# Optimization experiments

Hardware: AMD Instinct MI355X
Metric: run time of the kernel (lower is better)

## Reference

```python
import jax, jax.numpy as jnp
import numpy as np

B, T, C, H = 2, 2048, 1024, 16
HD = C // H  # head dim = 64


def setup_inputs() -> dict:
    key = jax.random.key(0)
    k0, k1, k2 = jax.random.split(key, 3)
    x = jax.random.normal(k0, (B, T, C), jnp.float32)
    W_attn = jax.random.normal(k1, (C, 3 * C), jnp.float32) * 0.02
    b_attn = jnp.zeros((3 * C,), jnp.float32)
    W_proj = jax.random.normal(k2, (C, C), jnp.float32) * 0.02
    b_proj = jnp.zeros((C,), jnp.float32)
    # causal mask, broadcast over (B, H) like torch masked_fill(~mask)
    attn_mask = jnp.tril(jnp.ones((T, T), dtype=bool))[None, None]
    return {"x": x, "W_attn": W_attn, "b_attn": b_attn,
            "W_proj": W_proj, "b_proj": b_proj, "attn_mask": attn_mask}


def _rotate_half(x):
    # interleaved rotate_half as in rotary-embedding-torch: (x1,x2)->(-x2,x1)
    x1 = x[..., 0::2]
    x2 = x[..., 1::2]
    return jnp.stack((-x2, x1), axis=-1).reshape(x.shape)


def _apply_rope(x):
    # x: [B, H, T, HD]
    hd = x.shape[-1]
    t = x.shape[-2]
    inv_freq = 1.0 / (10000.0 ** (jnp.arange(0, hd, 2, dtype=jnp.float32) / hd))
    freqs = jnp.arange(t, dtype=jnp.float32)[:, None] * inv_freq[None, :]  # [T, HD/2]
    freqs = jnp.repeat(freqs, 2, axis=-1)  # [T, HD], interleaved
    return x * jnp.cos(freqs) + _rotate_half(x) * jnp.sin(freqs)


def reference(x, W_attn, b_attn, W_proj, b_proj, attn_mask):
    Bb, Tt, Cc = x.shape
    qkv = x @ W_attn + b_attn                     # [B, T, 3C]
    q, k, v = jnp.split(qkv, 3, axis=-1)

    def to_heads(z):
        return z.reshape(Bb, Tt, H, HD).transpose(0, 2, 1, 3)  # [B, H, T, HD]

    q, k, v = to_heads(q), to_heads(k), to_heads(v)
    q = _apply_rope(q)
    k = _apply_rope(k)

    scale = 1.0 / jnp.sqrt(jnp.float32(HD))
    att = jnp.einsum('bhqd,bhkd->bhqk', q, k) * scale  # [B, H, T, T]
    att = jnp.where(attn_mask, att, jnp.float32(-10000.0))
    att = jax.nn.softmax(att, axis=-1)
    # dropout = 0.0 (eval): identity
    y = jnp.einsum('bhqk,bhkd->bhqd', att, v)           # [B, H, T, HD]
    y = y.transpose(0, 2, 1, 3).reshape(Bb, Tt, Cc)
    return y @ W_proj + b_proj
```

## Files before the change

### kernel.cpp

```cpp
#include <hip/hip_runtime.h>

#define B_ 2
#define T_ 2048
#define C_ 1024
#define H_ 16
#define HD_ 64

typedef unsigned short u16;
typedef unsigned int u32;
typedef __attribute__((ext_vector_type(8))) short short8;
typedef __attribute__((ext_vector_type(4))) float f32x4;
typedef __attribute__((ext_vector_type(2))) u32 uint2v;
typedef __attribute__((ext_vector_type(4))) u32 uint4v;

typedef __attribute__((address_space(1))) const void* as1cv;
typedef __attribute__((address_space(3))) void* as3v;

__device__ __forceinline__ u16 f2bf(float x){
  union { float f; u32 u; } v; v.f = x;
  u32 r = v.u + 0x7fffu + ((v.u >> 16) & 1u);
  return (u16)(r >> 16);
}
__device__ __forceinline__ float bf2f(u16 h){
  union { u32 u; float f; } v; v.u = ((u32)h) << 16;
  return v.f;
}
__device__ __forceinline__ u32 cvt_pk_bf16(float lo, float hi){
  u32 r;
  asm("v_cvt_pk_bf16_f32 %0, %1, %2" : "=v"(r) : "v"(lo), "v"(hi));
  return r;
}
__device__ __forceinline__ void gl_lds16(const u16* src, u16* dst){
  __builtin_amdgcn_global_load_lds((as1cv)src, (as3v)dst, 16, 0, 0);
}

__global__ void k_prep(const float* __restrict__ x, u16* __restrict__ xb,
                       const float* __restrict__ Wa, u16* __restrict__ WaT,
                       const float* __restrict__ Wp, u16* __restrict__ WpT)
{
  __shared__ float tile[32][33];
  int b = blockIdx.x;
  int tid = threadIdx.x;
  if (b < 4096){
    int i = b*256 + tid;
    f32x4 v = ((const f32x4*)x)[i];
    uint2v o;
    o.x = (u32)f2bf(v.x) | ((u32)f2bf(v.y) << 16);
    o.y = (u32)f2bf(v.z) | ((u32)f2bf(v.w) << 16);
    ((uint2v*)xb)[i] = o;
    return;
  }
  const float* in; u16* out; int R, Cc, c0, r0;
  if (b < 7168){
    int bb = b - 4096;
    in = Wa; out = WaT; R = 1024; Cc = 3072;
    c0 = (bb % 96) * 32; r0 = (bb / 96) * 32;
  } else {
    int bb = b - 7168;
    in = Wp; out = WpT; R = 1024; Cc = 1024;
    c0 = (bb & 31) * 32; r0 = (bb >> 5) * 32;
  }
  int tx = tid & 31, ty = tid >> 5;
#pragma unroll
  for (int ii = 0; ii < 4; ++ii)
    tile[ty + ii*8][tx] = in[(size_t)(r0 + ty + ii*8) * Cc + c0 + tx];
  __syncthreads();
#pragma unroll
  for (int ii = 0; ii < 4; ++ii)
    out[(size_t)(c0 + ty + ii*8) * R + r0 + tx] = f2bf(tile[tx][ty + ii*8]);
}

__global__ __launch_bounds__(256, 3)
void k_gemm0(const u16* __restrict__ A, const u16* __restrict__ Bt,
             const float* __restrict__ bias, u16* __restrict__ Qh,
             u16* __restrict__ Kh, u16* __restrict__ vt,
             int M, int N, int K)
{
  __shared__ u16 As[128*64];
  __shared__ u16 Bs[128*64];
  int nwg = gridDim.x;
  int cpx = nwg >> 3;
  int bid = blockIdx.x;
  int wg = (bid & 7) * cpx + (bid >> 3);
  int ntn = N >> 7;
  int m0 = (wg / ntn) << 7, n0 = (wg % ntn) << 7;
  int tid = threadIdx.x;
  int lane = tid & 63, w = tid >> 6;
  int c = lane & 15, g = lane >> 4;
  int wr = w >> 1, wc = w & 1;
  int c7 = c & 7;

  f32x4 z4 = {0.f,0.f,0.f,0.f};
  f32x4 acc[4][4];
#pragma unroll
  for (int i=0;i<4;++i)
#pragma unroll
    for (int j=0;j<4;++j) acc[i][j] = z4;

  u16* dstA = As + ((tid & 0xC0) << 3);
  u16* dstB = Bs + ((tid & 0xC0) << 3);
  int rowS[4], soffS[4];
#pragma unroll
  for (int it=0; it<4; ++it){
    int ch = it*256 + tid;
    rowS[it] = ch >> 3;
    soffS[it] = (((ch & 7) ^ (rowS[it] & 7)) << 3);
  }

  for (int k0 = 0; k0 < K; k0 += 64){
#pragma unroll
    for (int it = 0; it < 4; ++it)
      gl_lds16(A + (size_t)(m0+rowS[it])*K + k0 + soffS[it], dstA + it*2048);
#pragma unroll
    for (int it = 0; it < 4; ++it)
      gl_lds16(Bt + (size_t)(n0+rowS[it])*K + k0 + soffS[it], dstB + it*2048);
    __syncthreads();
#pragma unroll
    for (int ks = 0; ks < 2; ++ks){
      short8 af[4], bf[4];
      int sx = ((ks*4 + g) ^ c7) << 3;
#pragma unroll
      for (int i=0;i<4;++i)
        af[i] = *(const short8*)(As + (wr*64 + i*16 + c)*64 + sx);
#pragma unroll
      for (int j=0;j<4;++j)
        bf[j] = *(const short8*)(Bs + (wc*64 + j*16 + c)*64 + sx);
#pragma unroll
      for (int i=0;i<4;++i)
#pragma unroll
        for (int j=0;j<4;++j)
          acc[i][j] = __builtin_amdgcn_mfma_f32_16x16x32_bf16(af[i], bf[j], acc[i][j], 0, 0, 0);
    }
    __syncthreads();
  }

  if (n0 >= 2048){
#pragma unroll
    for (int i=0;i<4;++i){
      int rowb = m0 + wr*64 + i*16 + g*4;
      int bb = rowb >> 11, t0 = rowb & 2047;
#pragma unroll
      for (int j=0;j<4;++j){
        int col = n0 + wc*64 + j*16 + c;
        float bv = bias[col];
        int vc = col - 2048;
        int hh = vc >> 6, d = vc & 63;
        uint2v o;
        o.x = (u32)f2bf(acc[i][j].x + bv) | ((u32)f2bf(acc[i][j].y + bv) << 16);
        o.y = (u32)f2bf(acc[i][j].z + bv) | ((u32)f2bf(acc[i][j].w + bv) << 16);
        *(uint2v*)(vt + ((size_t)((bb*16 + hh)*64 + d))*2048 + t0) = o;
      }
    }
  } else {
    bool isQ = (n0 < 1024);
    u16* dsth = isQ ? Qh : Kh;
    int colb = isQ ? n0 : (n0 - 1024);
    float qsc = isQ ? 0.180336880f : 1.0f;
    float sgn = (c & 1) ? 1.f : -1.f;
#pragma unroll
    for (int nf=0; nf<4; ++nf){
      int scol = colb + wc*64 + nf*16 + c;
      int hh = scol >> 6, d = scol & 63;
      int ip = (d >> 1);
      float invr = exp2f((float)(-ip) * 0.4152410118609203f) * 0.15915494309f;
      float bv = bias[n0 + wc*64 + nf*16 + c];
      u16* base = dsth + (size_t)hh*2048*64 + d;
#pragma unroll
      for (int mf=0; mf<4; ++mf){
#pragma unroll
        for (int r=0; r<4; ++r){
          int row = m0 + wr*64 + mf*16 + g*4 + r;
          int t = row & 2047, b = row >> 11;
          float v = acc[mf][nf][r] + bv;
          float p = __shfl_xor(v, 1);
          float th = (float)t * invr;
          float fr = th - floorf(th);
          float sn = __builtin_amdgcn_sinf(fr);
          float cs = __builtin_amdgcn_cosf(fr);
          float y = (v*cs + p*sn*sgn) * qsc;
          base[((size_t)b*16*2048 + t)*64] = f2bf(y);
        }
      }
    }
  }
}

__global__ __launch_bounds__(256, 3)
void k_gemmp(const u16* __restrict__ A, const u16* __restrict__ Bt,
             const float* __restrict__ bias, float* __restrict__ outf)
{
  __shared__ u16 LDSG[24576];
  const int K = 1024, N = 1024;
  int nwg = gridDim.x;
  int cpx = nwg >> 3;
  int bid = blockIdx.x;
  int wg = (bid & 7) * cpx + (bid >> 3);
  int m0 = (wg >> 3) << 6, n0 = (wg & 7) << 7;
  int tid = threadIdx.x;
  int lane = tid & 63, w = tid >> 6;
  int c = lane & 15, g = lane >> 4;
  int wr = w >> 1, wc = w & 1;
  int c7 = c & 7;

  f32x4 z4 = {0.f,0.f,0.f,0.f};
  f32x4 acc[2][4];
#pragma unroll
  for (int i=0;i<2;++i)
#pragma unroll
    for (int j=0;j<4;++j) acc[i][j] = z4;

  int rowA[2], slotA[2], dstA[2];
#pragma unroll
  for (int it=0; it<2; ++it){
    int ch = it*256 + tid;
    rowA[it] = ch >> 3;
    slotA[it] = (((ch & 7) ^ (rowA[it] & 7)) << 3);
    dstA[it] = it*2048 + ((tid & 0xC0) << 3);
  }
  int rowB[4], slotB[4], dstB[4];
#pragma unroll
  for (int it=0; it<4; ++it){
    int ch = it*256 + tid;
    rowB[it] = ch >> 3;
    slotB[it] = (((ch & 7) ^ (rowB[it] & 7)) << 3);
    dstB[it] = 8192 + it*2048 + ((tid & 0xC0) << 3);
  }
  const u16* Abase = A + (size_t)m0*K;
  const u16* Bbase = Bt + (size_t)n0*K;

#pragma unroll
  for (int it=0; it<2; ++it)
    gl_lds16(Abase + (size_t)rowA[it]*K + slotA[it], LDSG + dstA[it]);
#pragma unroll
  for (int it=0; it<4; ++it)
    gl_lds16(Bbase + (size_t)rowB[it]*K + slotB[it], LDSG + dstB[it]);
  __syncthreads();

  const int nk = K >> 6;
  for (int kt = 0; kt < nk; ++kt){
    int cur = kt & 1;
    if (kt + 1 < nk){
      int k1 = (kt + 1) << 6;
      int nb = cur ^ 1;
#pragma unroll
      for (int it=0; it<2; ++it)
        gl_lds16(Abase + (size_t)rowA[it]*K + k1 + slotA[it], LDSG + nb*4096 + dstA[it]);
#pragma unroll
      for (int it=0; it<4; ++it)
        gl_lds16(Bbase + (size_t)rowB[it]*K + k1 + slotB[it], LDSG + nb*8192 + dstB[it]);
    }
    const u16* As = LDSG + cur*4096;
    const u16* Bs = LDSG + 8192 + cur*8192;
#pragma unroll
    for (int ks = 0; ks < 2; ++ks){
      short8 af[2], bf[4];
      int sx = ((ks*4 + g) ^ c7) << 3;
#pragma unroll
      for (int i=0;i<2;++i)
        af[i] = *(const short8*)(As + (wr*32 + i*16 + c)*64 + sx);
#pragma unroll
      for (int j=0;j<4;++j)
        bf[j] = *(const short8*)(Bs + (wc*64 + j*16 + c)*64 + sx);
#pragma unroll
      for (int i=0;i<2;++i)
#pragma unroll
        for (int j=0;j<4;++j)
          acc[i][j] = __builtin_amdgcn_mfma_f32_16x16x32_bf16(af[i], bf[j], acc[i][j], 0, 0, 0);
    }
    __syncthreads();
  }

#pragma unroll
  for (int i=0;i<2;++i){
#pragma unroll
    for (int j=0;j<4;++j){
      int col = n0 + wc*64 + j*16 + c;
      float bv = bias[col];
#pragma unroll
      for (int r=0;r<4;++r){
        int row = m0 + wr*32 + i*16 + g*4 + r;
        outf[(size_t)row*N + col] = acc[i][j][r] + bv;
      }
    }
  }
}

__global__ __launch_bounds__(256, 3)
void k_attn(const u16* __restrict__ Qh, const u16* __restrict__ Kh,
            const u16* __restrict__ Vt, u16* __restrict__ Pb,
            float* __restrict__ lp)
{
  __shared__ u16 KV[4*4096];
  __shared__ u16 Ps[4*32*64];

  int bid = blockIdx.x;
  int qt, ck, bh, l2nsp;
  if (bid < 1536){
    qt = 15 - (bid >> 7); ck = (bid >> 5) & 3; bh = bid & 31; l2nsp = 2;
  } else if (bid < 1728){
    int x = bid - 1536;
    qt = 3 - (x >> 6); ck = (x >> 5) & 1; bh = x & 31; l2nsp = 1;
  } else {
    qt = 0; ck = 0; bh = (bid - 1728) & 31; l2nsp = 0;
  }
  int q0 = qt << 7;
  int tid = threadIdx.x, lane = tid & 63, w = tid >> 6;
  int c = lane & 15, g = lane >> 4;
  int q0w = q0 + w*32;
  int nt = (qt + 1) << 1;
  int t0 = (nt * ck) >> l2nsp;
  int t1 = (nt * (ck + 1)) >> l2nsp;

  const u16* Kbase = Kh + (size_t)bh * T_ * 64;
  const u16* Vbase = Vt + (size_t)bh * 64 * T_;
  const u16* Qbase = Qh + (size_t)bh * T_ * 64;

  short8 qf[2][2];
#pragma unroll
  for (int qs=0;qs<2;++qs)
#pragma unroll
    for (int ks=0;ks<2;++ks)
      qf[qs][ks] = *(const short8*)(Qbase + (size_t)(q0w + qs*16 + c)*64 + ks*32 + g*8);

  f32x4 z4 = {0.f,0.f,0.f,0.f};
  f32x4 acc[2][4];
#pragma unroll
  for (int qs=0;qs<2;++qs)
#pragma unroll
    for (int ds=0;ds<4;++ds) acc[qs][ds] = z4;
  float psum[2] = {0.f, 0.f};

  char* PsB = (char*)Ps + w*4096;

  int row2[2], soff2[2];
  u16* dst0[2];
#pragma unroll
  for (int it=0; it<2; ++it){
    int ch = it*256 + tid;
    row2[it] = ch >> 3;
    int slot = ch & 7;
    soff2[it] = (slot ^ (row2[it] & 7)) << 3;
    dst0[it] = KV + ((it*256 + (tid & 0xC0)) << 3);
  }

  {
    int kv0 = t0 << 6;
#pragma unroll
    for (int it=0; it<2; ++it){
      gl_lds16(Kbase + (size_t)(kv0 + row2[it])*64 + soff2[it], dst0[it]);
      gl_lds16(Vbase + (size_t)row2[it]*T_ + kv0 + soff2[it], dst0[it] + 2*4096);
    }
  }
  __syncthreads();

  for (int t = t0; t < t1; ++t){
    int cur = (t - t0) & 1;
    int kv0 = t << 6;
    if (t + 1 < t1){
      int kvn = kv0 + 64;
      int nxt = cur ^ 1;
#pragma unroll
      for (int it=0; it<2; ++it){
        gl_lds16(Kbase + (size_t)(kvn + row2[it])*64 + soff2[it], dst0[it] + nxt*4096);
        gl_lds16(Vbase + (size_t)row2[it]*T_ + kvn + soff2[it], dst0[it] + (2+nxt)*4096);
      }
    }

    if (kv0 <= q0w + 31){
      const char* KsC = (const char*)(KV + cur*4096);
      const char* VsC = (const char*)(KV + (2+cur)*4096);

      f32x4 st[4][2];
#pragma unroll
      for (int kv=0;kv<4;++kv)
#pragma unroll
        for (int qs=0;qs<2;++qs) st[kv][qs] = z4;

#pragma unroll
      for (int ks=0;ks<2;++ks){
        short8 kf[4];
#pragma unroll
        for (int kv=0;kv<4;++kv){
          int row = kv*16 + c;
          kf[kv] = *(const short8*)(KsC + row*128 + (((ks*4+g) ^ (row&7)) << 4));
        }
#pragma unroll
        for (int kv=0;kv<4;++kv)
#pragma unroll
          for (int qs=0;qs<2;++qs)
            st[kv][qs] = __builtin_amdgcn_mfma_f32_16x16x32_bf16(kf[kv], qf[qs][ks], st[kv][qs], 0, 0, 0);
      }

      if (kv0 + 63 > q0w){
#pragma unroll
        for (int kv=0;kv<4;++kv)
#pragma unroll
          for (int qs=0;qs<2;++qs)
#pragma unroll
            for (int r=0;r<4;++r){
              int kvi = kv0 + kv*16 + g*4 + r;
              int qi = q0w + qs*16 + c;
              if (kvi > qi) st[kv][qs][r] = -INFINITY;
            }
      }

#pragma unroll
      for (int qs=0;qs<2;++qs){
        float s01 = 0.f, s23 = 0.f;
#pragma unroll
        for (int kv=0;kv<4;++kv){
          float e0 = __builtin_amdgcn_exp2f(st[kv][qs][0]);
          float e1 = __builtin_amdgcn_exp2f(st[kv][qs][1]);
          float e2 = __builtin_amdgcn_exp2f(st[kv][qs][2]);
          float e3 = __builtin_amdgcn_exp2f(st[kv][qs][3]);
          st[kv][qs][0] = e0; st[kv][qs][1] = e1;
          st[kv][qs][2] = e2; st[kv][qs][3] = e3;
          s01 += e0 + e1; s23 += e2 + e3;
        }
        psum[qs] += s01 + s23;
        int q = qs*16 + c;
#pragma unroll
        for (int kv=0;kv<4;++kv){
          uint2v o;
          o.x = cvt_pk_bf16(st[kv][qs][0], st[kv][qs][1]);
          o.y = cvt_pk_bf16(st[kv][qs][2], st[kv][qs][3]);
          *(uint2v*)(PsB + q*128 + ((kv*32 + g*8) ^ ((q&7) << 4))) = o;
        }
      }

#pragma unroll
      for (int ks=0;ks<2;++ks){
        short8 vb[4];
#pragma unroll
        for (int ds=0;ds<4;++ds){
          int row = ds*16 + c;
          vb[ds] = *(const short8*)(VsC + row*128 + (((ks*4+g) ^ (row&7)) << 4));
        }
#pragma unroll
        for (int qs=0;qs<2;++qs){
          int q = qs*16 + c;
          short8 pa = *(const short8*)(PsB + q*128 + (((ks*4+g) << 4) ^ ((q&7) << 4)));
#pragma unroll
          for (int ds=0;ds<4;++ds)
            acc[qs][ds] = __builtin_amdgcn_mfma_f32_16x16x32_bf16(pa, vb[ds], acc[qs][ds], 0, 0, 0);
        }
      }
    }

    __syncthreads();
  }

#pragma unroll
  for (int qs=0;qs<2;++qs){
    psum[qs] += __shfl_xor(psum[qs], 16);
    psum[qs] += __shfl_xor(psum[qs], 32);
  }
  if (g == 0){
    lp[ck*65536 + bh*2048 + q0w + c]      = psum[0];
    lp[ck*65536 + bh*2048 + q0w + 16 + c] = psum[1];
  }
#pragma unroll
  for (int qs=0;qs<2;++qs){
#pragma unroll
    for (int r=0;r<4;++r){
      int trow = q0w + qs*16 + g*4 + r;
      size_t off = (((size_t)(ck*32 + bh)*2048) + trow)*64;
#pragma unroll
      for (int ds=0;ds<4;++ds)
        Pb[off + ds*16 + c] = f2bf(acc[qs][ds][r]);
    }
  }
}

__global__ void k_merge(const u16* __restrict__ Pb, const float* __restrict__ lp,
                        u16* __restrict__ Y)
{
  int idx = blockIdx.x * 256 + threadIdx.x;
  int d8 = idx & 7;
  int t  = (idx >> 3) & 2047;
  int bh = idx >> 14;
  int qt = t >> 7;
  int lt = bh*2048 + t;
  float s[8];
  float l = lp[lt];
  {
    short8 p = *(const short8*)(Pb + (((size_t)bh*2048 + t) << 6) + d8*8);
#pragma unroll
    for (int j=0;j<8;++j) s[j] = bf2f((u16)p[j]);
  }
  if (qt >= 1){
    l += lp[lt + 65536];
    short8 p = *(const short8*)(Pb + (((size_t)(32 + bh)*2048 + t) << 6) + d8*8);
#pragma unroll
    for (int j=0;j<8;++j) s[j] += bf2f((u16)p[j]);
  }
  if (qt >= 4){
    l += lp[lt + 131072] + lp[lt + 196608];
    short8 p2 = *(const short8*)(Pb + (((size_t)(64 + bh)*2048 + t) << 6) + d8*8);
    short8 p3 = *(const short8*)(Pb + (((size_t)(96 + bh)*2048 + t) << 6) + d8*8);
#pragma unroll
    for (int j=0;j<8;++j) s[j] += bf2f((u16)p2[j]) + bf2f((u16)p3[j]);
  }
  float inv = 1.0f / l;
  uint4v o;
  o.x = cvt_pk_bf16(s[0]*inv, s[1]*inv);
  o.y = cvt_pk_bf16(s[2]*inv, s[3]*inv);
  o.z = cvt_pk_bf16(s[4]*inv, s[5]*inv);
  o.w = cvt_pk_bf16(s[6]*inv, s[7]*inv);
  int bb = bh >> 4, hh = bh & 15;
  *(uint4v*)(Y + ((size_t)(bb*2048 + t))*1024 + hh*64 + d8*8) = o;
}

extern "C" void kernel_launch(void* const* d_in, const int* in_sizes, int n_in,
                              void* d_out, int out_size, void* d_ws, size_t ws_size,
                              hipStream_t stream)
{
  const float* x  = (const float*)d_in[0];
  const float* Wa = (const float*)d_in[1];
  const float* ba = (const float*)d_in[2];
  const float* Wp = (const float*)d_in[3];
  const float* bp = (const float*)d_in[4];
  float* out = (float*)d_out;
  char* ws = (char*)d_ws;

  u16* xb  = (u16*)(ws);
  u16* WaT = (u16*)(ws + (8u  << 20));
  u16* Pb  = (u16*)(ws);
  u16* Qh  = (u16*)(ws + (32u << 20));
  u16* Y   = Qh;
  u16* Kh  = (u16*)(ws + (40u << 20));
  u16* Vt  = (u16*)(ws + (48u << 20));
  u16* WpT = (u16*)(ws + (56u << 20));
  float* lp = (float*)(ws + (58u << 20));

  k_prep<<<8192, 256, 0, stream>>>(x, xb, Wa, WaT, Wp, WpT);
  k_gemm0<<<768, 256, 0, stream>>>(xb, WaT, ba, Qh, Kh, Vt, 4096, 3072, 1024);
  k_attn<<<1760, 256, 0, stream>>>(Qh, Kh, Vt, Pb, lp);
  k_merge<<<2048, 256, 0, stream>>>(Pb, lp, Y);
  k_gemmp<<<512, 256, 0, stream>>>(Y, WpT, bp, out);
}
```

Before: 95.50 us.

## Fuse split-K attention merge into output projection GEMM A-tile loads

New measurement: 123.8 us. +29.6%, slower.

```diff
diff --git a/kernel.cpp b/kernel.cpp
--- a/kernel.cpp
+++ b/kernel.cpp
@@ -32,6 +32,42 @@
 }
 __device__ __forceinline__ void gl_lds16(const u16* src, u16* dst){
   __builtin_amdgcn_global_load_lds((as1cv)src, (as3v)dst, 16, 0, 0);
+}
+
+__device__ __forceinline__ short8 merge_a(const u16* __restrict__ Pb,
+                                          const float* __restrict__ lp,
+                                          int gr, int hh, int d0)
+{
+  int b = gr >> 11, t = gr & 2047;
+  int bh = b*16 + hh;
+  int qt = t >> 7;
+  int lt = bh*2048 + t;
+  size_t pbase = (((size_t)bh*2048) + t)*64 + d0;
+  float l = lp[lt];
+  float s[8];
+  short8 p = *(const short8*)(Pb + pbase);
+#pragma unroll
+  for (int j=0;j<8;++j) s[j] = bf2f((u16)p[j]);
+  if (qt >= 1){
+    l += lp[lt + 65536];
+    short8 p1 = *(const short8*)(Pb + pbase + 4194304u);
+#pragma unroll
+    for (int j=0;j<8;++j) s[j] += bf2f((u16)p1[j]);
+  }
+  if (qt >= 4){
+    l += lp[lt + 131072] + lp[lt + 196608];
+    short8 p2 = *(const short8*)(Pb + pbase + 8388608u);
+    short8 p3 = *(const short8*)(Pb + pbase + 12582912u);
+#pragma unroll
+    for (int j=0;j<8;++j) s[j] += bf2f((u16)p2[j]) + bf2f((u16)p3[j]);
+  }
+  float inv = 1.0f / l;
+  union { uint4v u; short8 s8; } cv;
+  cv.u.x = cvt_pk_bf16(s[0]*inv, s[1]*inv);
+  cv.u.y = cvt_pk_bf16(s[2]*inv, s[3]*inv);
+  cv.u.z = cvt_pk_bf16(s[4]*inv, s[5]*inv);
+  cv.u.w = cvt_pk_bf16(s[6]*inv, s[7]*inv);
+  return cv.s8;
 }
 
 __global__ void k_prep(const float* __restrict__ x, u16* __restrict__ xb,
@@ -186,8 +222,9 @@
 }
 
 __global__ __launch_bounds__(256, 3)
-void k_gemmp(const u16* __restrict__ A, const u16* __restrict__ Bt,
-             const float* __restrict__ bias, float* __restrict__ outf)
+void k_gemmp(const u16* __restrict__ Pb, const float* __restrict__ lp,
+             const u16* __restrict__ Bt, const float* __restrict__ bias,
+             float* __restrict__ outf)
 {
   __shared__ u16 LDSG[24576];
   const int K = 1024, N = 1024;
@@ -209,13 +246,13 @@
 #pragma unroll
     for (int j=0;j<4;++j) acc[i][j] = z4;
 
-  int rowA[2], slotA[2], dstA[2];
+  int rowA[2], slotA[2], grA[2];
 #pragma unroll
   for (int it=0; it<2; ++it){
     int ch = it*256 + tid;
     rowA[it] = ch >> 3;
     slotA[it] = (((ch & 7) ^ (rowA[it] & 7)) << 3);
-    dstA[it] = it*2048 + ((tid & 0xC0) << 3);
+    grA[it] = m0 + rowA[it];
   }
   int rowB[4], slotB[4], dstB[4];
 #pragma unroll
@@ -225,12 +262,13 @@
     slotB[it] = (((ch & 7) ^ (rowB[it] & 7)) << 3);
     dstB[it] = 8192 + it*2048 + ((tid & 0xC0) << 3);
   }
-  const u16* Abase = A + (size_t)m0*K;
   const u16* Bbase = Bt + (size_t)n0*K;
 
 #pragma unroll
-  for (int it=0; it<2; ++it)
-    gl_lds16(Abase + (size_t)rowA[it]*K + slotA[it], LDSG + dstA[it]);
+  for (int it=0; it<2; ++it){
+    short8 a0 = merge_a(Pb, lp, grA[it], 0, slotA[it]);
+    *(short8*)(LDSG + it*2048 + tid*8) = a0;
+  }
 #pragma unroll
   for (int it=0; it<4; ++it)
     gl_lds16(Bbase + (size_t)rowB[it]*K + slotB[it], LDSG + dstB[it]);
@@ -239,15 +277,17 @@
   const int nk = K >> 6;
   for (int kt = 0; kt < nk; ++kt){
     int cur = kt & 1;
-    if (kt + 1 < nk){
+    int nb = cur ^ 1;
+    short8 a_m[2];
+    bool have = (kt + 1 < nk);
+    if (have){
       int k1 = (kt + 1) << 6;
-      int nb = cur ^ 1;
-#pragma unroll
-      for (int it=0; it<2; ++it)
-        gl_lds16(Abase + (size_t)rowA[it]*K + k1 + slotA[it], LDSG + nb*4096 + dstA[it]);
 #pragma unroll
       for (int it=0; it<4; ++it)
         gl_lds16(Bbase + (size_t)rowB[it]*K + k1 + slotB[it], LDSG + nb*8192 + dstB[it]);
+#pragma unroll
+      for (int it=0; it<2; ++it)
+        a_m[it] = merge_a(Pb, lp, grA[it], kt + 1, slotA[it]);
     }
     const u16* As = LDSG + cur*4096;
     const u16* Bs = LDSG + 8192 + cur*8192;
@@ -266,6 +306,11 @@
 #pragma unroll
         for (int j=0;j<4;++j)
           acc[i][j] = __builtin_amdgcn_mfma_f32_16x16x32_bf16(af[i], bf[j], acc[i][j], 0, 0, 0);
+    }
+    if (have){
+#pragma unroll
+      for (int it=0; it<2; ++it)
+        *(short8*)(LDSG + nb*4096 + it*2048 + tid*8) = a_m[it];
     }
     __syncthreads();
   }
@@ -472,45 +517,6 @@
   }
 }
 
-__global__ void k_merge(const u16* __restrict__ Pb, const float* __restrict__ lp,
-                        u16* __restrict__ Y)
-{
-  int idx = blockIdx.x * 256 + threadIdx.x;
-  int d8 = idx & 7;
-  int t  = (idx >> 3) & 2047;
-  int bh = idx >> 14;
-  int qt = t >> 7;
-  int lt = bh*2048 + t;
-  float s[8];
-  float l = lp[lt];
-  {
-    short8 p = *(const short8*)(Pb + (((size_t)bh*2048 + t) << 6) + d8*8);
-#pragma unroll
-    for (int j=0;j<8;++j) s[j] = bf2f((u16)p[j]);
-  }
-  if (qt >= 1){
-    l += lp[lt + 65536];
-    short8 p = *(const short8*)(Pb + (((size_t)(32 + bh)*2048 + t) << 6) + d8*8);
-#pragma unroll
-    for (int j=0;j<8;++j) s[j] += bf2f((u16)p[j]);
-  }
-  if (qt >= 4){
-    l += lp[lt + 131072] + lp[lt + 196608];
-    short8 p2 = *(const short8*)(Pb + (((size_t)(64 + bh)*2048 + t) << 6) + d8*8);
-    short8 p3 = *(const short8*)(Pb + (((size_t)(96 + bh)*2048 + t) << 6) + d8*8);
-#pragma unroll
-    for (int j=0;j<8;++j) s[j] += bf2f((u16)p2[j]) + bf2f((u16)p3[j]);
-  }
-  float inv = 1.0f / l;
-  uint4v o;
-  o.x = cvt_pk_bf16(s[0]*inv, s[1]*inv);
-  o.y = cvt_pk_bf16(s[2]*inv, s[3]*inv);
-  o.z = cvt_pk_bf16(s[4]*inv, s[5]*inv);
-  o.w = cvt_pk_bf16(s[6]*inv, s[7]*inv);
-  int bb = bh >> 4, hh = bh & 15;
-  *(uint4v*)(Y + ((size_t)(bb*2048 + t))*1024 + hh*64 + d8*8) = o;
-}
-
 extern "C" void kernel_launch(void* const* d_in, const int* in_sizes, int n_in,
                               void* d_out, int out_size, void* d_ws, size_t ws_size,
                               hipStream_t stream)
@@ -527,7 +533,6 @@
   u16* WaT = (u16*)(ws + (8u  << 20));
   u16* Pb  = (u16*)(ws);
   u16* Qh  = (u16*)(ws + (32u << 20));
-  u16* Y   = Qh;
   u16* Kh  = (u16*)(ws + (40u << 20));
   u16* Vt  = (u16*)(ws + (48u << 20));
   u16* WpT = (u16*)(ws + (56u << 20));
@@ -536,6 +541,5 @@
   k_prep<<<8192, 256, 0, stream>>>(x, xb, Wa, WaT, Wp, WpT);
   k_gemm0<<<768, 256, 0, stream>>>(xb, WaT, ba, Qh, Kh, Vt, 4096, 3072, 1024);
   k_attn<<<1760, 256, 0, stream>>>(Qh, Kh, Vt, Pb, lp);
-  k_merge<<<2048, 256, 0, stream>>>(Pb, lp, Y);
-  k_gemmp<<<512, 256, 0, stream>>>(Y, WpT, bp, out);
-}
+  k_gemmp<<<512, 256, 0, stream>>>(Pb, lp, WpT, bp, out);
+}
```
